# Kernel optimization log

Measured on AMD Instinct MI355X. Metric: run time of the kernel, lower is better.

Reference implementation:

```python
import jax, jax.numpy as jnp
import numpy as np

H = 12          # num attention heads
DH = 64         # head dim
D = H * DH      # hidden size = 768
B, S = 2, 2048


def setup_inputs() -> dict:
    key = jax.random.key(0)
    ks = jax.random.split(key, 8)
    scale = 1.0 / np.sqrt(D)
    return {
        "hidden_states": jax.random.normal(ks[0], (B, S, D), jnp.float32),
        "attention_mask": jnp.zeros((B, 1, 1, S), jnp.float32),
        "position_bias": jax.random.normal(ks[1], (1, H, S, S), jnp.float32) * 0.1,
        "Wq": jax.random.normal(ks[2], (D, D), jnp.float32) * scale,
        "bq": jnp.zeros((D,), jnp.float32),
        "Wk": jax.random.normal(ks[3], (D, D), jnp.float32) * scale,
        "bk": jnp.zeros((D,), jnp.float32),
        "Wv": jax.random.normal(ks[4], (D, D), jnp.float32) * scale,
        "bv": jnp.zeros((D,), jnp.float32),
        "Wo": jax.random.normal(ks[5], (D, D), jnp.float32) * scale,
        "bo": jnp.zeros((D,), jnp.float32),
    }


def reference(hidden_states, attention_mask, position_bias,
              Wq, bq, Wk, bk, Wv, bv, Wo, bo):
    b, s, d = hidden_states.shape
    # Linear projections, then split heads: [B, S, D] -> [B, H, S, DH]
    def split_heads(x):
        return x.reshape(b, s, H, DH).transpose(0, 2, 1, 3)

    q = split_heads(hidden_states @ Wq.T + bq)
    k = split_heads(hidden_states @ Wk.T + bk)
    v = split_heads(hidden_states @ Wv.T + bv)

    # scores: [B, H, S, S]
    scores = jnp.einsum('bhqd,bhkd->bhqk', q, k) / jnp.sqrt(jnp.float32(DH))
    scores = scores + position_bias + attention_mask
    probs = jax.nn.softmax(scores, axis=-1)
    # dropout prob = 0.0 -> identity

    c = jnp.einsum('bhqk,bhkd->bhqd', probs, v)       # [B, H, S, DH]
    c = c.transpose(0, 2, 1, 3).reshape(b, s, d)      # [B, S, D]
    o = c @ Wo.T + bo
    return o
```

## Files before the change

kernel.cpp:

```cpp
#include <hip/hip_runtime.h>

typedef _Float16 f16x8 __attribute__((ext_vector_type(8)));
typedef float f32x4 __attribute__((ext_vector_type(4)));

#define NH 12
#define SEQ 2048
#define DM 768
#define DH 64

__global__ __launch_bounds__(256) void cast_kernel(
    const float* __restrict__ X, const float* __restrict__ Wq,
    const float* __restrict__ Wk, const float* __restrict__ Wv,
    const float* __restrict__ Wo, _Float16* __restrict__ Xh,
    _Float16* __restrict__ Wall)
{
    size_t base = ((size_t)blockIdx.x * 256 + threadIdx.x) * 8;
    const size_t NX = 3145728, NW = 589824, TOT = NX + 4 * NW;
    if (base >= TOT) return;
    const float* src;
    _Float16* dst;
    if (base < NX) { src = X + base; dst = Xh + base; }
    else {
        size_t r = base - NX;
        int w = (int)(r / NW);
        size_t o = r - (size_t)w * NW;
        src = (w == 0 ? Wq : w == 1 ? Wk : w == 2 ? Wv : Wo) + o;
        dst = Wall + r;
    }
    float4 a = *reinterpret_cast<const float4*>(src);
    float4 b = *reinterpret_cast<const float4*>(src + 4);
    f16x8 h;
    h[0] = (_Float16)a.x; h[1] = (_Float16)a.y; h[2] = (_Float16)a.z; h[3] = (_Float16)a.w;
    h[4] = (_Float16)b.x; h[5] = (_Float16)b.y; h[6] = (_Float16)b.z; h[7] = (_Float16)b.w;
    *reinterpret_cast<f16x8*>(dst) = h;
}

__global__ __launch_bounds__(256) void gemm_kernel(
    const _Float16* __restrict__ A,
    const _Float16* __restrict__ Wbase,
    const float* __restrict__ b0, const float* __restrict__ b1,
    const float* __restrict__ b2,
    _Float16* __restrict__ outQKV, float* __restrict__ outF32, int is_out)
{
    __shared__ _Float16 Asm[128 * 64];
    __shared__ _Float16 Bsm[128 * 64];
    const int tid = threadIdx.x;
    const int m0 = blockIdx.x * 128, n0 = blockIdx.y * 128, z = blockIdx.z;
    const _Float16* Wp = Wbase + (size_t)z * 589824;
    const float* bias = (z == 0) ? b0 : (z == 1 ? b1 : b2);
    const int w = tid >> 6, lane = tid & 63, lr = lane & 15, lg = lane >> 4;
    const int wm = w >> 1, wn = w & 1;

    f32x4 acc[4][4] = {};
    for (int kt = 0; kt < 12; ++kt) {
        __syncthreads();
        #pragma unroll
        for (int i = 0; i < 4; ++i) {
            int c = tid + i * 256;
            int row = c >> 3, col = (c & 7) * 8;
            int sw = (row & 7) << 4;
            f16x8 av = *reinterpret_cast<const f16x8*>(A + (size_t)(m0 + row) * 768 + kt * 64 + col);
            *reinterpret_cast<f16x8*>((char*)Asm + ((row * 128 + col * 2) ^ sw)) = av;
            f16x8 bv = *reinterpret_cast<const f16x8*>(Wp + (size_t)(n0 + row) * 768 + kt * 64 + col);
            *reinterpret_cast<f16x8*>((char*)Bsm + ((row * 128 + col * 2) ^ sw)) = bv;
        }
        __syncthreads();
        #pragma unroll
        for (int kf = 0; kf < 2; ++kf) {
            f16x8 af[4], bf[4];
            #pragma unroll
            for (int mi = 0; mi < 4; ++mi) {
                int row = wm * 64 + mi * 16 + lr;
                af[mi] = *reinterpret_cast<const f16x8*>(
                    (char*)Asm + ((row * 128 + kf * 64 + lg * 16) ^ ((row & 7) << 4)));
            }
            #pragma unroll
            for (int nj = 0; nj < 4; ++nj) {
                int row = wn * 64 + nj * 16 + lr;
                bf[nj] = *reinterpret_cast<const f16x8*>(
                    (char*)Bsm + ((row * 128 + kf * 64 + lg * 16) ^ ((row & 7) << 4)));
            }
            #pragma unroll
            for (int mi = 0; mi < 4; ++mi)
                #pragma unroll
                for (int nj = 0; nj < 4; ++nj)
                    acc[mi][nj] = __builtin_amdgcn_mfma_f32_16x16x32_f16(
                        af[mi], bf[nj], acc[mi][nj], 0, 0, 0);
        }
    }
    #pragma unroll
    for (int mi = 0; mi < 4; ++mi) {
        #pragma unroll
        for (int nj = 0; nj < 4; ++nj) {
            #pragma unroll
            for (int r = 0; r < 4; ++r) {
                int gm = m0 + wm * 64 + mi * 16 + lg * 4 + r;
                int gn = n0 + wn * 64 + nj * 16 + lr;
                float v = acc[mi][nj][r] + bias[gn];
                if (!is_out) {
                    int bb = gm >> 11, s = gm & 2047, hh = gn >> 6, dd = gn & 63;
                    outQKV[(size_t)z * 3145728 +
                           ((((size_t)bb * NH + hh) * SEQ + s) * DH + dd)] = (_Float16)v;
                } else {
                    outF32[(size_t)gm * 768 + gn] = v;
                }
            }
        }
    }
}

__global__ __launch_bounds__(256) void attn_kernel(
    const _Float16* __restrict__ Qh, const _Float16* __restrict__ Kh,
    const _Float16* __restrict__ Vh, const float* __restrict__ pb,
    const float* __restrict__ mask, _Float16* __restrict__ ctx)
{
    __shared__ _Float16 Kl[64 * 64];
    __shared__ _Float16 Vt[64 * 64];
    __shared__ _Float16 Pl[4 * 16 * 64];
    const int tid = threadIdx.x, w = tid >> 6, lane = tid & 63;
    const int lr = lane & 15, lg = lane >> 4;
    const int lin = blockIdx.x;
    const int xcd = lin & 7, idx = lin >> 3;
    const int bh = xcd * 3 + (idx >> 5);
    const int q0 = (idx & 31) << 6;
    const int h = bh % NH, b = bh / NH;
    const size_t headoff = ((size_t)b * NH + h) * SEQ * DH;
    const _Float16* Qp = Qh + headoff;
    const _Float16* Kp = Kh + headoff;
    const _Float16* Vp = Vh + headoff;
    const float L2E = 1.44269504f;

    f16x8 qf[2];
    #pragma unroll
    for (int kf = 0; kf < 2; ++kf)
        qf[kf] = *reinterpret_cast<const f16x8*>(
            Qp + (size_t)(q0 + w * 16 + lr) * DH + kf * 32 + lg * 8);

    const float* pbr[4];
    #pragma unroll
    for (int r = 0; r < 4; ++r)
        pbr[r] = pb + (size_t)h * SEQ * SEQ + (size_t)(q0 + w * 16 + lg * 4 + r) * SEQ;
    const float* mrow = mask + (size_t)b * SEQ;

    f32x4 oacc[4] = {};
    float m_r[4], l_r[4];
    #pragma unroll
    for (int r = 0; r < 4; ++r) { m_r[r] = -3.0e38f; l_r[r] = 0.f; }
    char* Pw = (char*)Pl + w * 2048;

    const int c0 = tid, c1 = tid + 256;
    const int row0 = c0 >> 3, col0 = (c0 & 7) << 3;
    const int row1 = c1 >> 3, col1 = (c1 & 7) << 3;
    f16x8 kn[2], vn[2];

    kn[0] = *reinterpret_cast<const f16x8*>(Kp + c0 * 8);
    kn[1] = *reinterpret_cast<const f16x8*>(Kp + c1 * 8);
    vn[0] = *reinterpret_cast<const f16x8*>(Vp + c0 * 8);
    vn[1] = *reinterpret_cast<const f16x8*>(Vp + c1 * 8);
    float pbc[4][4];
    #pragma unroll
    for (int cf = 0; cf < 4; ++cf) {
        float mk = mrow[cf * 16 + lr];
        #pragma unroll
        for (int r = 0; r < 4; ++r)
            pbc[cf][r] = (pbr[r][cf * 16 + lr] + mk) * L2E;
    }
    #pragma unroll
    for (int i = 0; i < 2; ++i) {
        int row = i ? row1 : row0, col = i ? col1 : col0;
        *reinterpret_cast<f16x8*>(
            (char*)Kl + ((row * 128 + col * 2) ^ ((row & 7) << 4))) = kn[i];
        #pragma unroll
        for (int j = 0; j < 8; ++j) {
            int d = col + j;
            *reinterpret_cast<_Float16*>(
                (char*)Vt + ((d * 128 + row * 2) ^ ((((d & 7) ^ ((d >> 3) & 7))) << 4))) = vn[i][j];
        }
    }
    __syncthreads();

    for (int kt0 = 0; kt0 < SEQ; kt0 += 64) {
        const int nt = (kt0 + 64 < SEQ) ? kt0 + 64 : kt0;
        kn[0] = *reinterpret_cast<const f16x8*>(Kp + (size_t)nt * DH + c0 * 8);
        kn[1] = *reinterpret_cast<const f16x8*>(Kp + (size_t)nt * DH + c1 * 8);
        vn[0] = *reinterpret_cast<const f16x8*>(Vp + (size_t)nt * DH + c0 * 8);
        vn[1] = *reinterpret_cast<const f16x8*>(Vp + (size_t)nt * DH + c1 * 8);
        float pbn[4][4];
        #pragma unroll
        for (int cf = 0; cf < 4; ++cf) {
            float mk = mrow[nt + cf * 16 + lr];
            #pragma unroll
            for (int r = 0; r < 4; ++r)
                pbn[cf][r] = (pbr[r][nt + cf * 16 + lr] + mk) * L2E;
        }

        f32x4 sc4[4] = {};
        #pragma unroll
        for (int cf = 0; cf < 4; ++cf) {
            #pragma unroll
            for (int kf = 0; kf < 2; ++kf) {
                f16x8 kb = *reinterpret_cast<const f16x8*>(
                    (char*)Kl + (((cf * 16 + lr) * 128 + kf * 64 + lg * 16) ^ ((lr & 7) << 4)));
                sc4[cf] = __builtin_amdgcn_mfma_f32_16x16x32_f16(qf[kf], kb, sc4[cf], 0, 0, 0);
            }
        }
        float sv[4][4];
        #pragma unroll
        for (int cf = 0; cf < 4; ++cf)
            #pragma unroll
            for (int r = 0; r < 4; ++r)
                sv[cf][r] = sc4[cf][r] * 0.18033688f + pbc[cf][r];

        float rs[4], scale[4];
        #pragma unroll
        for (int r = 0; r < 4; ++r) {
            float t = fmaxf(fmaxf(sv[0][r], sv[1][r]), fmaxf(sv[2][r], sv[3][r]));
            #pragma unroll
            for (int msk = 1; msk < 16; msk <<= 1) t = fmaxf(t, __shfl_xor(t, msk));
            float mn = fmaxf(m_r[r], t);
            scale[r] = exp2f(m_r[r] - mn);
            m_r[r] = mn;
            rs[r] = 0.f;
        }
        #pragma unroll
        for (int cf = 0; cf < 4; ++cf)
            #pragma unroll
            for (int r = 0; r < 4; ++r) {
                float p = exp2f(sv[cf][r] - m_r[r]);
                rs[r] += p;
                int prow = lg * 4 + r;
                *reinterpret_cast<_Float16*>(
                    Pw + ((prow * 128 + (cf * 16 + lr) * 2) ^ ((prow & 7) << 4))) = (_Float16)p;
            }
        #pragma unroll
        for (int r = 0; r < 4; ++r) {
            #pragma unroll
            for (int msk = 1; msk < 16; msk <<= 1) rs[r] += __shfl_xor(rs[r], msk);
            l_r[r] = l_r[r] * scale[r] + rs[r];
        }
        #pragma unroll
        for (int cf = 0; cf < 4; ++cf)
            #pragma unroll
            for (int r = 0; r < 4; ++r) oacc[cf][r] *= scale[r];

        #pragma unroll
        for (int kf = 0; kf < 2; ++kf) {
            f16x8 pa = *reinterpret_cast<const f16x8*>(
                Pw + ((lr * 128 + kf * 64 + lg * 16) ^ ((lr & 7) << 4)));
            #pragma unroll
            for (int cf = 0; cf < 4; ++cf) {
                int d = cf * 16 + lr;
                f16x8 vb = *reinterpret_cast<const f16x8*>(
                    (char*)Vt + ((d * 128 + kf * 64 + lg * 16) ^ ((((d & 7) ^ ((d >> 3) & 7))) << 4)));
                oacc[cf] = __builtin_amdgcn_mfma_f32_16x16x32_f16(pa, vb, oacc[cf], 0, 0, 0);
            }
        }

        __syncthreads();
        #pragma unroll
        for (int i = 0; i < 2; ++i) {
            int row = i ? row1 : row0, col = i ? col1 : col0;
            *reinterpret_cast<f16x8*>(
                (char*)Kl + ((row * 128 + col * 2) ^ ((row & 7) << 4))) = kn[i];
            #pragma unroll
            for (int j = 0; j < 8; ++j) {
                int d = col + j;
                *reinterpret_cast<_Float16*>(
                    (char*)Vt + ((d * 128 + row * 2) ^ ((((d & 7) ^ ((d >> 3) & 7))) << 4))) = vn[i][j];
            }
        }
        #pragma unroll
        for (int cf = 0; cf < 4; ++cf)
            #pragma unroll
            for (int r = 0; r < 4; ++r) pbc[cf][r] = pbn[cf][r];
        __syncthreads();
    }

    #pragma unroll
    for (int r = 0; r < 4; ++r) {
        float inv = 1.0f / l_r[r];
        int grow = q0 + w * 16 + lg * 4 + r;
        #pragma unroll
        for (int cf = 0; cf < 4; ++cf)
            ctx[((size_t)b * SEQ + grow) * DM + h * DH + cf * 16 + lr] =
                (_Float16)(oacc[cf][r] * inv);
    }
}

extern "C" void kernel_launch(void* const* d_in, const int* in_sizes, int n_in,
                              void* d_out, int out_size, void* d_ws, size_t ws_size,
                              hipStream_t stream) {
    const float* X    = (const float*)d_in[0];
    const float* mask = (const float*)d_in[1];
    const float* pb   = (const float*)d_in[2];
    const float* Wq   = (const float*)d_in[3];
    const float* bq   = (const float*)d_in[4];
    const float* Wk   = (const float*)d_in[5];
    const float* bk   = (const float*)d_in[6];
    const float* Wv   = (const float*)d_in[7];
    const float* bv   = (const float*)d_in[8];
    const float* Wo   = (const float*)d_in[9];
    const float* bo   = (const float*)d_in[10];
    float* out = (float*)d_out;

    _Float16* Xh   = (_Float16*)d_ws;
    _Float16* Wall = Xh + 3145728;
    _Float16* QKV  = Wall + 4 * 589824;
    _Float16* ctx  = QKV + 3 * 3145728;

    cast_kernel<<<2688, 256, 0, stream>>>(X, Wq, Wk, Wv, Wo, Xh, Wall);
    gemm_kernel<<<dim3(32, 6, 3), 256, 0, stream>>>(
        Xh, Wall, bq, bk, bv, QKV, nullptr, 0);
    attn_kernel<<<768, 256, 0, stream>>>(
        QKV, QKV + 3145728, QKV + 2 * 3145728, pb, mask, ctx);
    gemm_kernel<<<dim3(32, 6, 1), 256, 0, stream>>>(
        ctx, Wall + 3 * 589824, bo, bo, bo, nullptr, out, 1);
}
```

Before: 192.1 us.

## Split attention along the key dimension into two halves with a merge kernel

The attention kernel now splits each head's key range into two halves, doubling the grid from 768 to 1536 blocks. Each block writes an unnormalized fp16 partial output plus its running max and sum. A new merge kernel combines the two halves with log-sum-exp rescaling and writes the context. This is meant to fill the 256 CUs better than 768 blocks did, at the cost of an extra launch, partial-output traffic, and fp16 rounding of unnormalized accumulators.

```diff
diff --git a/kernel.cpp b/kernel.cpp
--- a/kernel.cpp
+++ b/kernel.cpp
@@ -7,6 +7,7 @@
 #define SEQ 2048
 #define DM 768
 #define DH 64
+#define NROWS 49152
 
 __global__ __launch_bounds__(256) void cast_kernel(
     const float* __restrict__ X, const float* __restrict__ Wq,
@@ -112,7 +113,8 @@
 __global__ __launch_bounds__(256) void attn_kernel(
     const _Float16* __restrict__ Qh, const _Float16* __restrict__ Kh,
     const _Float16* __restrict__ Vh, const float* __restrict__ pb,
-    const float* __restrict__ mask, _Float16* __restrict__ ctx)
+    const float* __restrict__ mask, _Float16* __restrict__ Opart,
+    float* __restrict__ ml)
 {
     __shared__ _Float16 Kl[64 * 64];
     __shared__ _Float16 Vt[64 * 64];
@@ -121,8 +123,12 @@
     const int lr = lane & 15, lg = lane >> 4;
     const int lin = blockIdx.x;
     const int xcd = lin & 7, idx = lin >> 3;
-    const int bh = xcd * 3 + (idx >> 5);
-    const int q0 = (idx & 31) << 6;
+    const int bh = xcd * 3 + (idx >> 6);
+    const int rem = idx & 63;
+    const int q0 = (rem >> 1) << 6;
+    const int ks = rem & 1;
+    const int kbase = ks << 10;
+    const int kend = kbase + 1024;
     const int h = bh % NH, b = bh / NH;
     const size_t headoff = ((size_t)b * NH + h) * SEQ * DH;
     const _Float16* Qp = Qh + headoff;
@@ -153,17 +159,17 @@
     const int row1 = c1 >> 3, col1 = (c1 & 7) << 3;
     f16x8 kn[2], vn[2];
 
-    kn[0] = *reinterpret_cast<const f16x8*>(Kp + c0 * 8);
-    kn[1] = *reinterpret_cast<const f16x8*>(Kp + c1 * 8);
-    vn[0] = *reinterpret_cast<const f16x8*>(Vp + c0 * 8);
-    vn[1] = *reinterpret_cast<const f16x8*>(Vp + c1 * 8);
+    kn[0] = *reinterpret_cast<const f16x8*>(Kp + (size_t)kbase * DH + c0 * 8);
+    kn[1] = *reinterpret_cast<const f16x8*>(Kp + (size_t)kbase * DH + c1 * 8);
+    vn[0] = *reinterpret_cast<const f16x8*>(Vp + (size_t)kbase * DH + c0 * 8);
+    vn[1] = *reinterpret_cast<const f16x8*>(Vp + (size_t)kbase * DH + c1 * 8);
     float pbc[4][4];
     #pragma unroll
     for (int cf = 0; cf < 4; ++cf) {
-        float mk = mrow[cf * 16 + lr];
+        float mk = mrow[kbase + cf * 16 + lr];
         #pragma unroll
         for (int r = 0; r < 4; ++r)
-            pbc[cf][r] = (pbr[r][cf * 16 + lr] + mk) * L2E;
+            pbc[cf][r] = (pbr[r][kbase + cf * 16 + lr] + mk) * L2E;
     }
     #pragma unroll
     for (int i = 0; i < 2; ++i) {
@@ -179,8 +185,8 @@
     }
     __syncthreads();
 
-    for (int kt0 = 0; kt0 < SEQ; kt0 += 64) {
-        const int nt = (kt0 + 64 < SEQ) ? kt0 + 64 : kt0;
+    for (int kt0 = kbase; kt0 < kend; kt0 += 64) {
+        const int nt = (kt0 + 64 < kend) ? kt0 + 64 : kt0;
         kn[0] = *reinterpret_cast<const f16x8*>(Kp + (size_t)nt * DH + c0 * 8);
         kn[1] = *reinterpret_cast<const f16x8*>(Kp + (size_t)nt * DH + c1 * 8);
         vn[0] = *reinterpret_cast<const f16x8*>(Vp + (size_t)nt * DH + c0 * 8);
@@ -278,13 +284,41 @@
 
     #pragma unroll
     for (int r = 0; r < 4; ++r) {
-        float inv = 1.0f / l_r[r];
         int grow = q0 + w * 16 + lg * 4 + r;
-        #pragma unroll
-        for (int cf = 0; cf < 4; ++cf)
-            ctx[((size_t)b * SEQ + grow) * DM + h * DH + cf * 16 + lr] =
-                (_Float16)(oacc[cf][r] * inv);
-    }
+        size_t rowi = ((size_t)b * NH + h) * SEQ + grow;
+        _Float16* od = Opart + ((size_t)ks * NROWS + rowi) * DH;
+        #pragma unroll
+        for (int cf = 0; cf < 4; ++cf)
+            od[cf * 16 + lr] = (_Float16)oacc[cf][r];
+        if (lr == 0) {
+            ml[rowi * 4 + ks * 2 + 0] = m_r[r];
+            ml[rowi * 4 + ks * 2 + 1] = l_r[r];
+        }
+    }
+}
+
+__global__ __launch_bounds__(256) void merge_kernel(
+    const _Float16* __restrict__ Opart, const float* __restrict__ ml,
+    _Float16* __restrict__ ctx)
+{
+    int gid = blockIdx.x * 256 + threadIdx.x;
+    int row = gid >> 3, d8 = (gid & 7) << 3;
+    const size_t NP = (size_t)NROWS * DH;
+    f16x8 o0 = *reinterpret_cast<const f16x8*>(Opart + (size_t)row * DH + d8);
+    f16x8 o1 = *reinterpret_cast<const f16x8*>(Opart + NP + (size_t)row * DH + d8);
+    float4 m = *reinterpret_cast<const float4*>(ml + (size_t)row * 4);
+    float M = fmaxf(m.x, m.z);
+    float a0 = exp2f(m.x - M), a1 = exp2f(m.z - M);
+    float inv = 1.0f / (a0 * m.y + a1 * m.w);
+    a0 *= inv; a1 *= inv;
+    f16x8 o;
+    #pragma unroll
+    for (int j = 0; j < 8; ++j)
+        o[j] = (_Float16)(a0 * (float)o0[j] + a1 * (float)o1[j]);
+    int b = row / (NH * SEQ);
+    int hs = row - b * (NH * SEQ);
+    int h = hs >> 11, s = hs & 2047;
+    *reinterpret_cast<f16x8*>(ctx + ((size_t)b * SEQ + s) * DM + h * DH + d8) = o;
 }
 
 extern "C" void kernel_launch(void* const* d_in, const int* in_sizes, int n_in,
@@ -303,16 +337,19 @@
     const float* bo   = (const float*)d_in[10];
     float* out = (float*)d_out;
 
-    _Float16* Xh   = (_Float16*)d_ws;
-    _Float16* Wall = Xh + 3145728;
-    _Float16* QKV  = Wall + 4 * 589824;
-    _Float16* ctx  = QKV + 3 * 3145728;
+    _Float16* Xh    = (_Float16*)d_ws;
+    _Float16* Wall  = Xh + 3145728;
+    _Float16* QKV   = Wall + 4 * 589824;
+    _Float16* ctx   = QKV + 3 * 3145728;
+    _Float16* Opart = ctx + 3145728;
+    float*    ml    = (float*)(Opart + 2 * 3145728);
 
     cast_kernel<<<2688, 256, 0, stream>>>(X, Wq, Wk, Wv, Wo, Xh, Wall);
     gemm_kernel<<<dim3(32, 6, 3), 256, 0, stream>>>(
         Xh, Wall, bq, bk, bv, QKV, nullptr, 0);
-    attn_kernel<<<768, 256, 0, stream>>>(
-        QKV, QKV + 3145728, QKV + 2 * 3145728, pb, mask, ctx);
+    attn_kernel<<<1536, 256, 0, stream>>>(
+        QKV, QKV + 3145728, QKV + 2 * 3145728, pb, mask, Opart, ml);
+    merge_kernel<<<1536, 256, 0, stream>>>(Opart, ml, ctx);
     gemm_kernel<<<dim3(32, 6, 1), 256, 0, stream>>>(
         ctx, Wall + 3 * 589824, bo, bo, bo, nullptr, out, 1);
 }
```

Result: no change. 190.2 us (-1.0%).
